# Kernel tuning notes

Measured on AMD Instinct MI355X. Metric: run time of the kernel, lower is better.

## Reference

```python
import jax, jax.numpy as jnp
import numpy as np

N_LAYERS = 8
D_MODEL = 64
D_STATE = 32
D_CONV = 4
D_INNER = 128          # expand * d_model
HEADDIM = 64
NHEADS = D_INNER // HEADDIM      # 2
CONV_DIM = D_INNER + 2 * D_STATE # 192 (x, B, C)
D_IN_PROJ = 2 * D_INNER + 2 * D_STATE + NHEADS  # 322
EPS = 1e-5


def setup_inputs() -> dict:
    key = jax.random.key(0)
    ks = jax.random.split(key, 8)
    x = jax.random.normal(ks[0], (16, 4096, D_MODEL), dtype=jnp.float32)
    Win = jax.random.normal(ks[1], (N_LAYERS, D_MODEL, D_IN_PROJ), dtype=jnp.float32) * 0.05
    conv_w = jax.random.normal(ks[2], (N_LAYERS, CONV_DIM, D_CONV), dtype=jnp.float32) * 0.2
    conv_b = jnp.zeros((N_LAYERS, CONV_DIM), dtype=jnp.float32)
    dt_bias = jax.random.uniform(ks[3], (N_LAYERS, NHEADS), minval=-4.0, maxval=-1.0)
    A_log = jnp.log(jax.random.uniform(ks[4], (N_LAYERS, NHEADS), minval=1.0, maxval=16.0))
    Dp = jnp.ones((N_LAYERS, NHEADS), dtype=jnp.float32)
    norm_w = jnp.ones((N_LAYERS, D_INNER), dtype=jnp.float32)
    Wout = jax.random.normal(ks[5], (N_LAYERS, D_INNER, D_MODEL), dtype=jnp.float32) * 0.05
    return {"x": x, "Win": Win, "conv_w": conv_w, "conv_b": conv_b,
            "dt_bias": dt_bias, "A_log": A_log, "Dp": Dp,
            "norm_w": norm_w, "Wout": Wout}


def _mamba2_layer(u, Win, conv_w, conv_b, dt_bias, A_log, Dp, norm_w, Wout):
    b, l, _ = u.shape
    zxbcdt = u @ Win                                   # (b,l,322)
    z = zxbcdt[..., :D_INNER]                          # gate (b,l,128)
    xBC = zxbcdt[..., D_INNER:D_INNER + CONV_DIM]      # (b,l,192)
    dt = jax.nn.softplus(zxbcdt[..., D_INNER + CONV_DIM:] + dt_bias)  # (b,l,H)

    # causal depthwise conv over time, then SiLU
    xc = jnp.pad(xBC.transpose(0, 2, 1), ((0, 0), (0, 0), (D_CONV - 1, 0)))
    xc = jax.lax.conv_general_dilated(
        xc, conv_w[:, None, :], (1,), 'VALID',
        feature_group_count=CONV_DIM,
        dimension_numbers=('NCH', 'OIH', 'NCH'))
    xBC = jax.nn.silu((xc + conv_b[None, :, None]).transpose(0, 2, 1))  # (b,l,192)

    xs = xBC[..., :D_INNER].reshape(b, l, NHEADS, HEADDIM)   # (b,l,h,p)
    B = xBC[..., D_INNER:D_INNER + D_STATE]                  # (b,l,n)
    C = xBC[..., D_INNER + D_STATE:]                         # (b,l,n)

    A = -jnp.exp(A_log)                                      # (h,) negative
    dA = jnp.exp(dt * A)                                     # (b,l,h)

    # sequential selective scan over time; state (b,h,p,n)
    def step(hst, inp):
        dA_t, dt_t, x_t, B_t, C_t = inp
        hst = hst * dA_t[:, :, None, None] + \
              (dt_t[:, :, None] * x_t)[..., None] * B_t[:, None, None, :]
        y_t = jnp.einsum('bhpn,bn->bhp', hst, C_t)
        return hst, y_t

    h0 = jnp.zeros((b, NHEADS, HEADDIM, D_STATE), dtype=u.dtype)
    seq = (jnp.moveaxis(dA, 1, 0), jnp.moveaxis(dt, 1, 0),
           jnp.moveaxis(xs, 1, 0), jnp.moveaxis(B, 1, 0), jnp.moveaxis(C, 1, 0))
    _, ys = jax.lax.scan(step, h0, seq)                      # (l,b,h,p)
    y = jnp.moveaxis(ys, 0, 1) + Dp[None, None, :, None] * xs  # (b,l,h,p)
    y = y.reshape(b, l, D_INNER)

    # gated RMSNorm (norm_before_gate=False): normalize after gating
    y = y * jax.nn.silu(z)
    y = y * jax.lax.rsqrt(jnp.mean(y * y, axis=-1, keepdims=True) + EPS) * norm_w
    return y @ Wout                                          # (b,l,d_model)


def reference(x, Win, conv_w, conv_b, dt_bias, A_log, Dp, norm_w, Wout):
    h = x
    for i in range(N_LAYERS - 1):
        h = _mamba2_layer(h, Win[i], conv_w[i], conv_b[i], dt_bias[i],
                          A_log[i], Dp[i], norm_w[i], Wout[i])
    h = jax.lax.stop_gradient(h)  # layers[:-1] run under torch.no_grad()
    i = N_LAYERS - 1
    return _mamba2_layer(h, Win[i], conv_w[i], conv_b[i], dt_bias[i],
                         A_log[i], Dp[i], norm_w[i], Wout[i])
```

## Files before the change

### kernel.cpp

```cpp
#include <hip/hip_runtime.h>
#include <math.h>

#define BATCH   16
#define SEQ     4096
#define DMODEL  64
#define DINNER  128
#define DSTATE  32
#define NHEADS  2
#define HEADDIM 64
#define CONVDIM 192
#define PROJ    322
#define QC      64
#define NCHUNK  (SEQ/QC)
#define BL      (BATCH*SEQ)
#define NPAD    336

typedef __attribute__((ext_vector_type(8))) short short8;
typedef __attribute__((ext_vector_type(4))) float f32x4;

__device__ inline unsigned short f2b(float f){
  union { float f; unsigned u; } v; v.f = f;
  unsigned r = v.u + 0x7FFF + ((v.u >> 16) & 1);
  return (unsigned short)(r >> 16);
}
__device__ inline float b2f(unsigned short s){
  union { unsigned u; float f; } v; v.u = ((unsigned)s) << 16; return v.f;
}
__device__ inline void split2(float x, unsigned short& h, unsigned short& l){
  unsigned short hh = f2b(x);
  h = hh;
  l = f2b(x - b2f(hh));
}

__device__ float g_z   [(size_t)BL*DINNER];
__device__ float g_xbc [(size_t)BL*CONVDIM];
__device__ float g_y   [(size_t)BL*DINNER];
__device__ unsigned short g_C[(size_t)BL*DSTATE];
__device__ float g_dt  [BATCH*NHEADS*SEQ];
__device__ float g_cum [BATCH*NHEADS*SEQ];
__device__ float g_ctot[BATCH*NHEADS*NCHUNK];
__device__ float g_S   [BATCH*NHEADS*NCHUNK*DSTATE*HEADDIM];
__device__ float g_H   [BATCH*NHEADS*NCHUNK*DSTATE*HEADDIM];
__device__ float g_ping0[(size_t)BL*DMODEL];
__device__ float g_ping1[(size_t)BL*DMODEL];
__device__ unsigned short g_WinTh [8*NPAD*DMODEL];
__device__ unsigned short g_WinTl [8*NPAD*DMODEL];
__device__ unsigned short g_WoutTh[8*DMODEL*DINNER];
__device__ unsigned short g_WoutTl[8*DMODEL*DINNER];

__global__ __launch_bounds__(256) void k_prep(const float* __restrict__ Win,
                                              const float* __restrict__ Wout,
                                              const float* __restrict__ normw) {
  const int idx = blockIdx.x*256 + threadIdx.x;
  const int NW = 8*NPAD*DMODEL;
  if (idx < NW) {
    int layer = idx / (NPAD*DMODEL);
    int rem   = idx - layer*(NPAD*DMODEL);
    int n = rem >> 6, k = rem & 63;
    float v = (n < PROJ) ? Win[(size_t)layer*DMODEL*PROJ + k*PROJ + n] : 0.f;
    split2(v, g_WinTh[idx], g_WinTl[idx]);
  } else {
    int i2 = idx - NW;
    if (i2 < 8*DMODEL*DINNER) {
      int layer = i2 / (DMODEL*DINNER);
      int rem   = i2 - layer*(DMODEL*DINNER);
      int n = rem >> 7, k = rem & 127;
      float v = Wout[(size_t)layer*DINNER*DMODEL + k*DMODEL + n] * normw[layer*DINNER + k];
      split2(v, g_WoutTh[i2], g_WoutTl[i2]);
    }
  }
}

__global__ __launch_bounds__(256) void k_inproj(const float* __restrict__ xext, int sel,
                                                const unsigned short* __restrict__ WinTh,
                                                const unsigned short* __restrict__ WinTl,
                                                const float* __restrict__ Win,
                                                const float* __restrict__ dt_bias,
                                                const float* __restrict__ A_log) {
  __shared__ float stgAll[4][16][68];
  const float* __restrict__ X = (sel==0) ? xext : (sel==1 ? g_ping0 : g_ping1);
  const int bx = blockIdx.x;
  const int chunk = bx >> 1, half = bx & 1;
  const int row0 = chunk * 64;
  const int tid = threadIdx.x;
  const int w = tid>>6, l = tid&63, lane15 = l&15, quad = l>>4;

  const float* xrow = &X[(size_t)(row0 + 16*w + lane15)*DMODEL + quad*8];
  float4 f0 = *(const float4*)(xrow);
  float4 f1 = *(const float4*)(xrow + 4);
  float4 f2 = *(const float4*)(xrow + 32);
  float4 f3 = *(const float4*)(xrow + 36);

  if (half==0 && w < 2) {
    const int h = w, t = l;
    float acc = 0.f;
    const float* xr = &X[(size_t)(row0+t)*DMODEL];
#pragma unroll
    for (int k=0;k<64;k++) acc = fmaf(xr[k], Win[k*PROJ + (DINNER+CONVDIM) + h], acc);
    float xv = acc + dt_bias[h];
    float dtv = (xv > 20.f) ? xv : log1pf(expf(xv));
    float A = -expf(A_log[h]);
    float cum = dtv * A;
#pragma unroll
    for (int off=1; off<64; off<<=1){
      float v = __shfl_up(cum, off);
      if (t >= off) cum += v;
    }
    const int b = chunk>>6, ch = chunk&63;
    const int base = (b*NHEADS + h)*SEQ + ch*QC + t;
    g_dt [base] = dtv;
    g_cum[base] = cum;
    if (t == 63) g_ctot[(b*NHEADS+h)*NCHUNK + ch] = cum;
  }

  short8 a0h, a0l, a1h, a1l;
  {
    float v0[8] = {f0.x,f0.y,f0.z,f0.w,f1.x,f1.y,f1.z,f1.w};
    float v1[8] = {f2.x,f2.y,f2.z,f2.w,f3.x,f3.y,f3.z,f3.w};
    unsigned short hh, ll;
#pragma unroll
    for (int j=0;j<8;j++){ split2(v0[j], hh, ll); a0h[j]=(short)hh; a0l[j]=(short)ll; }
#pragma unroll
    for (int j=0;j<8;j++){ split2(v1[j], hh, ll); a1h[j]=(short)hh; a1l[j]=(short)ll; }
  }

  float (*stg)[68] = stgAll[w];
  const int gS = (half==0) ? 0 : 2;
  const int gE = (half==0) ? 2 : 5;
#pragma unroll 1
  for (int g5=gS; g5<gE; g5++){
    f32x4 acc4[4];
#pragma unroll
    for (int tt=0; tt<4; tt++){
      int t = g5*4 + tt;
      const unsigned short* bph = &WinTh[(16*t + lane15)*64 + quad*8];
      const unsigned short* bpl = &WinTl[(16*t + lane15)*64 + quad*8];
      short8 b0h = *(const short8*)bph;
      short8 b1h = *(const short8*)(bph + 32);
      short8 b0l = *(const short8*)bpl;
      short8 b1l = *(const short8*)(bpl + 32);
      f32x4 acc = {0.f,0.f,0.f,0.f};
      acc = __builtin_amdgcn_mfma_f32_16x16x32_bf16(a0h, b0h, acc, 0, 0, 0);
      acc = __builtin_amdgcn_mfma_f32_16x16x32_bf16(a1h, b1h, acc, 0, 0, 0);
      acc = __builtin_amdgcn_mfma_f32_16x16x32_bf16(a0l, b0h, acc, 0, 0, 0);
      acc = __builtin_amdgcn_mfma_f32_16x16x32_bf16(a1l, b1h, acc, 0, 0, 0);
      acc = __builtin_amdgcn_mfma_f32_16x16x32_bf16(a0h, b0l, acc, 0, 0, 0);
      acc = __builtin_amdgcn_mfma_f32_16x16x32_bf16(a1h, b1l, acc, 0, 0, 0);
      acc4[tt] = acc;
    }
#pragma unroll
    for (int tt=0; tt<4; tt++)
#pragma unroll
      for (int r=0;r<4;r++)
        stg[quad*4+r][tt*16+lane15] = acc4[tt][r];
#pragma unroll
    for (int it=0; it<4; it++){
      int e = it*64 + l;
      int lr = e>>4, c4 = (e&15)<<2;
      float4 v = *(const float4*)&stg[lr][c4];
      size_t grow = row0 + 16*w + lr;
      int gcol = g5*64 + c4;
      if (g5 < 2) *(float4*)&g_z  [grow*DINNER  + gcol]          = v;
      else        *(float4*)&g_xbc[grow*CONVDIM + gcol - DINNER] = v;
    }
  }
}

__global__ __launch_bounds__(256,4) void k_chunkA(const float* __restrict__ conv_w,
                                                  const float* __restrict__ conv_b,
                                                  const float* __restrict__ Dp) {
  __shared__ float Xf[64][66];
  __shared__ unsigned short Xt [64][72];
  __shared__ unsigned short Bt [32][72];
  union BCG {
    struct { unsigned short Bsh[64][40]; unsigned short Csh[64][40]; } bc;
    unsigned short Gsh[64][72];
  };
  __shared__ BCG u;
  const int bx = blockIdx.x; const int b = bx>>7, h=(bx>>6)&1, ch=bx&63;
  const int tid = threadIdx.x;
  const size_t row0 = (size_t)b*SEQ + (size_t)ch*QC;
  const int cbase = (b*NHEADS+h)*SEQ + ch*QC;
  const float dph = Dp[h];
  if (tid < QC){
    float cl = g_cum[cbase+63];
    float cu = g_cum[cbase+tid], dtv = g_dt[cbase+tid];
    Xf[tid][64] = cu;
    Xf[tid][65] = dtv;
    ((float*)&Bt[tid>>1][64])[tid&1] = expf(cl - cu) * dtv;
  }
  const int cc = tid & 127, half = tid >> 7, t0 = half*32;
  const int gch = (cc < 64) ? (h*64 + cc) : (64 + cc);
  const float w0 = conv_w[gch*4+0], w1 = conv_w[gch*4+1], w2 = conv_w[gch*4+2], w3 = conv_w[gch*4+3];
  const float bb = conv_b[gch];
  float v0, v1, v2;
  if (ch==0 && half==0){ v0=0.f; v1=0.f; v2=0.f; }
  else {
    v0 = g_xbc[(row0+t0-3)*CONVDIM + gch];
    v1 = g_xbc[(row0+t0-2)*CONVDIM + gch];
    v2 = g_xbc[(row0+t0-1)*CONVDIM + gch];
  }
  __syncthreads();
  if (cc < 64){
#pragma unroll
    for (int blk=0; blk<4; ++blk){
      unsigned short xb[8];
#pragma unroll
      for (int j=0;j<8;j++){
        int t = t0 + blk*8 + j;
        float v3 = g_xbc[(row0+t)*CONVDIM + gch];
        float a = fmaf(w0,v0, fmaf(w1,v1, fmaf(w2,v2, fmaf(w3,v3, bb))));
        float sv = a / (1.f + expf(-a));
        Xf[cc][t] = sv;
        xb[j] = f2b(sv);
        v0=v1; v1=v2; v2=v3;
      }
      *(short8*)&Xt[cc][t0 + blk*8] = *(const short8*)xb;
    }
  } else if (cc < 96){
    const int n = cc - 64;
#pragma unroll
    for (int blk=0; blk<4; ++blk){
      unsigned short bt8[8];
#pragma unroll
      for (int j=0;j<8;j++){
        int t = t0 + blk*8 + j;
        float v3 = g_xbc[(row0+t)*CONVDIM + gch];
        float a = fmaf(w0,v0, fmaf(w1,v1, fmaf(w2,v2, fmaf(w3,v3, bb))));
        float sv = a / (1.f + expf(-a));
        u.bc.Bsh[t][n] = f2b(sv);
        float ew = ((const float*)&Bt[t>>1][64])[t&1];
        bt8[j] = f2b(sv * ew);
        v0=v1; v1=v2; v2=v3;
      }
      *(short8*)&Bt[n][t0 + blk*8] = *(const short8*)bt8;
    }
  } else {
    const int n = cc - 96;
#pragma unroll 4
    for (int t=t0; t<t0+32; t++){
      float v3 = g_xbc[(row0+t)*CONVDIM + gch];
      float a = fmaf(w0,v0, fmaf(w1,v1, fmaf(w2,v2, fmaf(w3,v3, bb))));
      float sv = a / (1.f + expf(-a));
      u.bc.Csh[t][n] = f2b(sv);
      if (h == 0) g_C[(row0+t)*DSTATE + n] = f2b(sv);
      v0=v1; v1=v2; v2=v3;
    }
  }
  __syncthreads();
  const int w = tid>>6, l = tid&63, lane15 = l&15, quad = l>>4;
  short8 afr = *(const short8*)&u.bc.Csh[16*w + lane15][quad*8];
  f32x4 gacc[4];
#pragma unroll
  for (int tn=0;tn<4;tn++){
    short8 bfr = *(const short8*)&u.bc.Bsh[16*tn + lane15][quad*8];
    f32x4 z = {0.f,0.f,0.f,0.f};
    gacc[tn] = __builtin_amdgcn_mfma_f32_16x16x32_bf16(afr, bfr, z, 0, 0, 0);
  }
  __syncthreads();
#pragma unroll
  for (int tn=0;tn<4;tn++){
    int s = 16*tn + lane15;
    float cs = Xf[s][64], ds = Xf[s][65];
#pragma unroll
    for (int r=0;r<4;r++){
      int t = 16*w + quad*4 + r;
      float gv = 0.f;
      if (s <= t) gv = expf(Xf[t][64]-cs) * ds * gacc[tn][r];
      u.Gsh[t][s] = f2b(gv);
    }
  }
  __syncthreads();
#pragma unroll
  for (int tn=0;tn<4;tn++){
    f32x4 acc = {0.f,0.f,0.f,0.f};
#pragma unroll
    for (int ks=0;ks<2;ks++){
      short8 a  = *(const short8*)&u.Gsh[16*w  + lane15][quad*8 + 32*ks];
      short8 bf = *(const short8*)&Xt [16*tn + lane15][quad*8 + 32*ks];
      acc = __builtin_amdgcn_mfma_f32_16x16x32_bf16(a, bf, acc, 0, 0, 0);
    }
    int p = 16*tn + lane15;
#pragma unroll
    for (int r=0;r<4;r++){
      int t = 16*w + quad*4 + r;
      g_y[(row0+t)*DINNER + h*HEADDIM + p] = acc[r] + dph * Xf[p][t];
    }
  }
  const size_t sb = (size_t)((b*NHEADS+h)*NCHUNK + ch) * (DSTATE*HEADDIM);
  const int tm2 = w & 1, tnb = (w>>1)*2;
#pragma unroll
  for (int tt=0;tt<2;tt++){
    int tn2 = tnb + tt;
    f32x4 acc = {0.f,0.f,0.f,0.f};
#pragma unroll
    for (int ks=0;ks<2;ks++){
      short8 a  = *(const short8*)&Bt[16*tm2 + lane15][quad*8 + 32*ks];
      short8 bf = *(const short8*)&Xt[16*tn2 + lane15][quad*8 + 32*ks];
      acc = __builtin_amdgcn_mfma_f32_16x16x32_bf16(a, bf, acc, 0, 0, 0);
    }
    int p = 16*tn2 + lane15;
#pragma unroll
    for (int r=0;r<4;r++){
      int n = 16*tm2 + quad*4 + r;
      g_S[sb + n*HEADDIM + p] = acc[r];
    }
  }
}

__global__ __launch_bounds__(256) void k_chunkScan() {
  __shared__ float dAc[NCHUNK];
  const int idx = blockIdx.x*256 + threadIdx.x;
  const int np = idx & 2047;
  const int bh = idx >> 11;
  if (threadIdx.x < NCHUNK) dAc[threadIdx.x] = expf(g_ctot[bh*NCHUNK + threadIdx.x]);
  __syncthreads();
  float h = 0.f;
  const size_t base = (size_t)bh*NCHUNK*2048 + np;
#pragma unroll 1
  for (int k0=0; k0<NCHUNK; k0+=8){
    float s[8];
#pragma unroll
    for (int j=0;j<8;j++) s[j] = g_S[base + (size_t)(k0+j)*2048];
    float hs[8];
#pragma unroll
    for (int j=0;j<8;j++){
      hs[j] = h;
      h = h*dAc[k0+j] + s[j];
    }
#pragma unroll
    for (int j=0;j<8;j++) g_H[base + (size_t)(k0+j)*2048] = hs[j];
  }
}

__global__ __launch_bounds__(256,3) void k_fusedC(const unsigned short* __restrict__ WoutTh,
                                                  const unsigned short* __restrict__ WoutTl,
                                                  float* __restrict__ dout, int dsel) {
  __shared__ float Cl[QC][DSTATE+1];
  __shared__ float ec[NHEADS][QC];
  __shared__ unsigned short yAh[64][136];
  __shared__ unsigned short yAl[64][136];
  float* __restrict__ out = (dsel==0) ? g_ping0 : (dsel==1 ? g_ping1 : dout);
  const int bx = blockIdx.x; const int b = bx>>6, ch = bx&63;
  const int tid = threadIdx.x;
  const size_t row0 = (size_t)b*SEQ + (size_t)ch*QC;
  const int w = tid>>6, l = tid&63, lane15 = l&15, quad = l>>4;
#pragma unroll
  for (int j=0;j<8;j++){ int e=tid+j*256; int s=e>>5, n=e&31;
    Cl[s][n] = b2f(g_C[(row0+s)*DSTATE + n]); }
  if (tid < 128){ int h_=tid>>6, s=tid&63;
    ec[h_][s] = expf(g_cum[(b*NHEADS+h_)*SEQ + ch*QC + s]); }
  float hr[64];
  {
    const float* H0 = &g_H[(size_t)((b*NHEADS+0)*NCHUNK + ch)*2048];
    const float* H1 = &g_H[(size_t)((b*NHEADS+1)*NCHUNK + ch)*2048];
#pragma unroll
    for (int n=0;n<32;n++){ hr[n] = H0[n*64 + l]; hr[32+n] = H1[n*64 + l]; }
  }
  __syncthreads();
#pragma unroll 1
  for (int i=0;i<16;i++){
    const int r = 16*w + i;
    const size_t row = row0 + r;
    float d0 = 0.f, d1 = 0.f;
#pragma unroll
    for (int n=0;n<32;n++){
      float c = Cl[r][n];
      d0 = fmaf(c, hr[n],    d0);
      d1 = fmaf(c, hr[32+n], d1);
    }
    float yv0 = g_y[row*DINNER + l]      + ec[0][r]*d0;
    float yv1 = g_y[row*DINNER + l + 64] + ec[1][r]*d1;
    float z0 = g_z[row*DINNER + l];
    float z1 = g_z[row*DINNER + l + 64];
    yv0 *= z0 / (1.f + expf(-z0));
    yv1 *= z1 / (1.f + expf(-z1));
    float ss = yv0*yv0 + yv1*yv1;
#pragma unroll
    for (int off=32; off>=1; off>>=1) ss += __shfl_xor(ss, off);
    float sc = rsqrtf(ss*(1.f/128.f) + 1e-5f);
    split2(yv0*sc, yAh[r][l],    yAl[r][l]);
    split2(yv1*sc, yAh[r][l+64], yAl[r][l+64]);
  }
  __syncthreads();
  short8 afh[4], afl[4];
#pragma unroll
  for (int ks=0;ks<4;ks++){
    afh[ks] = *(const short8*)&yAh[16*w + lane15][quad*8 + 32*ks];
    afl[ks] = *(const short8*)&yAl[16*w + lane15][quad*8 + 32*ks];
  }
  __syncthreads();
  float (*stgF)[68] = (float(*)[68])((float*)&yAh[0][0] + (size_t)w*16*68);
#pragma unroll
  for (int tc=0;tc<4;tc++){
    f32x4 acc = {0.f,0.f,0.f,0.f};
#pragma unroll
    for (int ks=0;ks<4;ks++){
      const unsigned short* bph = &WoutTh[(16*tc + lane15)*DINNER + quad*8 + 32*ks];
      const unsigned short* bpl = &WoutTl[(16*tc + lane15)*DINNER + quad*8 + 32*ks];
      short8 bh  = *(const short8*)bph;
      short8 blo = *(const short8*)bpl;
      acc = __builtin_amdgcn_mfma_f32_16x16x32_bf16(afh[ks], bh,  acc, 0, 0, 0);
      acc = __builtin_amdgcn_mfma_f32_16x16x32_bf16(afl[ks], bh,  acc, 0, 0, 0);
      acc = __builtin_amdgcn_mfma_f32_16x16x32_bf16(afh[ks], blo, acc, 0, 0, 0);
    }
#pragma unroll
    for (int r=0;r<4;r++)
      stgF[quad*4+r][tc*16+lane15] = acc[r];
  }
#pragma unroll
  for (int it=0; it<4; it++){
    int e = it*64 + l;
    int lr = e>>4, c4 = (e&15)<<2;
    float4 v = *(const float4*)&stgF[lr][c4];
    *(float4*)&out[(row0 + 16*w + lr)*DMODEL + c4] = v;
  }
}

extern "C" void kernel_launch(void* const* d_in, const int* in_sizes, int n_in,
                              void* d_out, int out_size, void* d_ws, size_t ws_size,
                              hipStream_t stream) {
  (void)in_sizes; (void)n_in; (void)d_ws; (void)ws_size; (void)out_size;
  const float* x       = (const float*)d_in[0];
  const float* Win     = (const float*)d_in[1];
  const float* conv_w  = (const float*)d_in[2];
  const float* conv_b  = (const float*)d_in[3];
  const float* dt_bias = (const float*)d_in[4];
  const float* A_log   = (const float*)d_in[5];
  const float* Dp      = (const float*)d_in[6];
  const float* norm_w  = (const float*)d_in[7];
  const float* Wout    = (const float*)d_in[8];

  k_prep<<<(8*(NPAD*DMODEL + DMODEL*DINNER) + 255)/256, 256, 0, stream>>>(Win, Wout, norm_w);

  unsigned short *winTh, *winTl, *woutTh, *woutTl;
  hipGetSymbolAddress((void**)&winTh,  HIP_SYMBOL(g_WinTh));
  hipGetSymbolAddress((void**)&winTl,  HIP_SYMBOL(g_WinTl));
  hipGetSymbolAddress((void**)&woutTh, HIP_SYMBOL(g_WoutTh));
  hipGetSymbolAddress((void**)&woutTl, HIP_SYMBOL(g_WoutTl));

  for (int layer = 0; layer < 8; ++layer) {
    const int insel = (layer==0) ? 0 : ((((layer-1)&1)==0) ? 1 : 2);
    const int dsel  = (layer==7) ? 2 : ((layer&1)==0 ? 0 : 1);

    k_inproj<<<(BL/64)*2, 256, 0, stream>>>(x, insel,
                                        winTh + (size_t)layer*NPAD*DMODEL,
                                        winTl + (size_t)layer*NPAD*DMODEL,
                                        Win + (size_t)layer*DMODEL*PROJ,
                                        dt_bias + layer*NHEADS, A_log + layer*NHEADS);
    k_chunkA<<<BATCH*NHEADS*NCHUNK, 256, 0, stream>>>(conv_w + (size_t)layer*CONVDIM*4,
                                                      conv_b + (size_t)layer*CONVDIM,
                                                      Dp + layer*NHEADS);
    k_chunkScan<<<(BATCH*NHEADS*DSTATE*HEADDIM)/256, 256, 0, stream>>>();
    k_fusedC<<<BATCH*NCHUNK, 256, 0, stream>>>(woutTh + (size_t)layer*DMODEL*DINNER,
                                               woutTl + (size_t)layer*DMODEL*DINNER,
                                               (float*)d_out, dsel);
  }
}
```

Baseline: 1.275 ms.

## Fuse input projection into chunk kernel, recomputing conv halo to drop xBC buffer

Merges the in-projection GEMM with the conv/chunk-state kernel, so each (batch, head, chunk) block computes its own x/B/C projection slices into shared memory. The 3-row conv halo is taken from the previous chunk by recomputing a 16-row projection tile. This removes the global round trip through the g_xbc buffer and one kernel launch. In exchange, B/C and the halo rows are recomputed per head, occupancy drops to 2 blocks per CU, and shared memory use grows.

```diff
diff --git a/kernel.cpp b/kernel.cpp
--- a/kernel.cpp
+++ b/kernel.cpp
@@ -33,7 +33,6 @@
 }
 
 __device__ float g_z   [(size_t)BL*DINNER];
-__device__ float g_xbc [(size_t)BL*CONVDIM];
 __device__ float g_y   [(size_t)BL*DINNER];
 __device__ unsigned short g_C[(size_t)BL*DSTATE];
 __device__ float g_dt  [BATCH*NHEADS*SEQ];
@@ -71,104 +70,16 @@
   }
 }
 
-__global__ __launch_bounds__(256) void k_inproj(const float* __restrict__ xext, int sel,
-                                                const unsigned short* __restrict__ WinTh,
-                                                const unsigned short* __restrict__ WinTl,
-                                                const float* __restrict__ Win,
-                                                const float* __restrict__ dt_bias,
-                                                const float* __restrict__ A_log) {
-  __shared__ float stgAll[4][16][68];
-  const float* __restrict__ X = (sel==0) ? xext : (sel==1 ? g_ping0 : g_ping1);
-  const int bx = blockIdx.x;
-  const int chunk = bx >> 1, half = bx & 1;
-  const int row0 = chunk * 64;
-  const int tid = threadIdx.x;
-  const int w = tid>>6, l = tid&63, lane15 = l&15, quad = l>>4;
-
-  const float* xrow = &X[(size_t)(row0 + 16*w + lane15)*DMODEL + quad*8];
-  float4 f0 = *(const float4*)(xrow);
-  float4 f1 = *(const float4*)(xrow + 4);
-  float4 f2 = *(const float4*)(xrow + 32);
-  float4 f3 = *(const float4*)(xrow + 36);
-
-  if (half==0 && w < 2) {
-    const int h = w, t = l;
-    float acc = 0.f;
-    const float* xr = &X[(size_t)(row0+t)*DMODEL];
-#pragma unroll
-    for (int k=0;k<64;k++) acc = fmaf(xr[k], Win[k*PROJ + (DINNER+CONVDIM) + h], acc);
-    float xv = acc + dt_bias[h];
-    float dtv = (xv > 20.f) ? xv : log1pf(expf(xv));
-    float A = -expf(A_log[h]);
-    float cum = dtv * A;
-#pragma unroll
-    for (int off=1; off<64; off<<=1){
-      float v = __shfl_up(cum, off);
-      if (t >= off) cum += v;
-    }
-    const int b = chunk>>6, ch = chunk&63;
-    const int base = (b*NHEADS + h)*SEQ + ch*QC + t;
-    g_dt [base] = dtv;
-    g_cum[base] = cum;
-    if (t == 63) g_ctot[(b*NHEADS+h)*NCHUNK + ch] = cum;
-  }
-
-  short8 a0h, a0l, a1h, a1l;
-  {
-    float v0[8] = {f0.x,f0.y,f0.z,f0.w,f1.x,f1.y,f1.z,f1.w};
-    float v1[8] = {f2.x,f2.y,f2.z,f2.w,f3.x,f3.y,f3.z,f3.w};
-    unsigned short hh, ll;
-#pragma unroll
-    for (int j=0;j<8;j++){ split2(v0[j], hh, ll); a0h[j]=(short)hh; a0l[j]=(short)ll; }
-#pragma unroll
-    for (int j=0;j<8;j++){ split2(v1[j], hh, ll); a1h[j]=(short)hh; a1l[j]=(short)ll; }
-  }
-
-  float (*stg)[68] = stgAll[w];
-  const int gS = (half==0) ? 0 : 2;
-  const int gE = (half==0) ? 2 : 5;
-#pragma unroll 1
-  for (int g5=gS; g5<gE; g5++){
-    f32x4 acc4[4];
-#pragma unroll
-    for (int tt=0; tt<4; tt++){
-      int t = g5*4 + tt;
-      const unsigned short* bph = &WinTh[(16*t + lane15)*64 + quad*8];
-      const unsigned short* bpl = &WinTl[(16*t + lane15)*64 + quad*8];
-      short8 b0h = *(const short8*)bph;
-      short8 b1h = *(const short8*)(bph + 32);
-      short8 b0l = *(const short8*)bpl;
-      short8 b1l = *(const short8*)(bpl + 32);
-      f32x4 acc = {0.f,0.f,0.f,0.f};
-      acc = __builtin_amdgcn_mfma_f32_16x16x32_bf16(a0h, b0h, acc, 0, 0, 0);
-      acc = __builtin_amdgcn_mfma_f32_16x16x32_bf16(a1h, b1h, acc, 0, 0, 0);
-      acc = __builtin_amdgcn_mfma_f32_16x16x32_bf16(a0l, b0h, acc, 0, 0, 0);
-      acc = __builtin_amdgcn_mfma_f32_16x16x32_bf16(a1l, b1h, acc, 0, 0, 0);
-      acc = __builtin_amdgcn_mfma_f32_16x16x32_bf16(a0h, b0l, acc, 0, 0, 0);
-      acc = __builtin_amdgcn_mfma_f32_16x16x32_bf16(a1h, b1l, acc, 0, 0, 0);
-      acc4[tt] = acc;
-    }
-#pragma unroll
-    for (int tt=0; tt<4; tt++)
-#pragma unroll
-      for (int r=0;r<4;r++)
-        stg[quad*4+r][tt*16+lane15] = acc4[tt][r];
-#pragma unroll
-    for (int it=0; it<4; it++){
-      int e = it*64 + l;
-      int lr = e>>4, c4 = (e&15)<<2;
-      float4 v = *(const float4*)&stg[lr][c4];
-      size_t grow = row0 + 16*w + lr;
-      int gcol = g5*64 + c4;
-      if (g5 < 2) *(float4*)&g_z  [grow*DINNER  + gcol]          = v;
-      else        *(float4*)&g_xbc[grow*CONVDIM + gcol - DINNER] = v;
-    }
-  }
-}
-
-__global__ __launch_bounds__(256,4) void k_chunkA(const float* __restrict__ conv_w,
-                                                  const float* __restrict__ conv_b,
-                                                  const float* __restrict__ Dp) {
+__global__ __launch_bounds__(256,2) void k_fusedAB(const float* __restrict__ xext, int sel,
+                                                   const unsigned short* __restrict__ WinTh,
+                                                   const unsigned short* __restrict__ WinTl,
+                                                   const float* __restrict__ Win,
+                                                   const float* __restrict__ dt_bias,
+                                                   const float* __restrict__ A_log,
+                                                   const float* __restrict__ conv_w,
+                                                   const float* __restrict__ conv_b,
+                                                   const float* __restrict__ Dp) {
+  __shared__ float PC[80][66];
   __shared__ float Xf[64][66];
   __shared__ unsigned short Xt [64][72];
   __shared__ unsigned short Bt [32][72];
@@ -177,38 +88,115 @@
     unsigned short Gsh[64][72];
   };
   __shared__ BCG u;
-  const int bx = blockIdx.x; const int b = bx>>7, h=(bx>>6)&1, ch=bx&63;
+
+  const float* __restrict__ X = (sel==0) ? xext : (sel==1 ? g_ping0 : g_ping1);
+  const int bx = blockIdx.x; const int b = bx>>7, h = (bx>>6)&1, ch = bx&63;
   const int tid = threadIdx.x;
+  const int w = tid>>6, l = tid&63, lane15 = l&15, quad = l>>4;
   const size_t row0 = (size_t)b*SEQ + (size_t)ch*QC;
   const int cbase = (b*NHEADS+h)*SEQ + ch*QC;
   const float dph = Dp[h];
-  if (tid < QC){
-    float cl = g_cum[cbase+63];
-    float cu = g_cum[cbase+tid], dtv = g_dt[cbase+tid];
-    Xf[tid][64] = cu;
-    Xf[tid][65] = dtv;
-    ((float*)&Bt[tid>>1][64])[tid&1] = expf(cl - cu) * dtv;
-  }
-  const int cc = tid & 127, half = tid >> 7, t0 = half*32;
-  const int gch = (cc < 64) ? (h*64 + cc) : (64 + cc);
-  const float w0 = conv_w[gch*4+0], w1 = conv_w[gch*4+1], w2 = conv_w[gch*4+2], w3 = conv_w[gch*4+3];
-  const float bb = conv_b[gch];
-  float v0, v1, v2;
-  if (ch==0 && half==0){ v0=0.f; v1=0.f; v2=0.f; }
-  else {
-    v0 = g_xbc[(row0+t0-3)*CONVDIM + gch];
-    v1 = g_xbc[(row0+t0-2)*CONVDIM + gch];
-    v2 = g_xbc[(row0+t0-1)*CONVDIM + gch];
-  }
-  __syncthreads();
-  if (cc < 64){
-#pragma unroll
-    for (int blk=0; blk<4; ++blk){
+
+  const float* xrow = &X[(row0 + 16*w + lane15)*DMODEL + quad*8];
+  float4 f0 = *(const float4*)(xrow);
+  float4 f1 = *(const float4*)(xrow + 4);
+  float4 f2 = *(const float4*)(xrow + 32);
+  float4 f3 = *(const float4*)(xrow + 36);
+  short8 a0h, a0l, a1h, a1l;
+  {
+    float v0[8] = {f0.x,f0.y,f0.z,f0.w,f1.x,f1.y,f1.z,f1.w};
+    float v1[8] = {f2.x,f2.y,f2.z,f2.w,f3.x,f3.y,f3.z,f3.w};
+    unsigned short hh, ll;
+#pragma unroll
+    for (int j=0;j<8;j++){ split2(v0[j], hh, ll); a0h[j]=(short)hh; a0l[j]=(short)ll; }
+#pragma unroll
+    for (int j=0;j<8;j++){ split2(v1[j], hh, ll); a1h[j]=(short)hh; a1l[j]=(short)ll; }
+  }
+  short8 e0h, e0l, e1h, e1l;
+  if (ch != 0){
+    const float* xh = &X[(row0 - 16 + lane15)*DMODEL + quad*8];
+    float4 g0 = *(const float4*)(xh);
+    float4 g1 = *(const float4*)(xh + 4);
+    float4 g2 = *(const float4*)(xh + 32);
+    float4 g3 = *(const float4*)(xh + 36);
+    float v0[8] = {g0.x,g0.y,g0.z,g0.w,g1.x,g1.y,g1.z,g1.w};
+    float v1[8] = {g2.x,g2.y,g2.z,g2.w,g3.x,g3.y,g3.z,g3.w};
+    unsigned short hh, ll;
+#pragma unroll
+    for (int j=0;j<8;j++){ split2(v0[j], hh, ll); e0h[j]=(short)hh; e0l[j]=(short)ll; }
+#pragma unroll
+    for (int j=0;j<8;j++){ split2(v1[j], hh, ll); e1h[j]=(short)hh; e1l[j]=(short)ll; }
+  }
+
+  if (w == 0) {
+    const int t = l;
+    float acc = 0.f;
+    const float* xr = &X[(row0+t)*DMODEL];
+#pragma unroll
+    for (int k=0;k<64;k++) acc = fmaf(xr[k], Win[k*PROJ + (DINNER+CONVDIM) + h], acc);
+    float xv = acc + dt_bias[h];
+    float dtv = (xv > 20.f) ? xv : log1pf(expf(xv));
+    float A = -expf(A_log[h]);
+    float cum = dtv * A;
+#pragma unroll
+    for (int off=1; off<64; off<<=1){
+      float v = __shfl_up(cum, off);
+      if (t >= off) cum += v;
+    }
+    g_dt [cbase+t] = dtv;
+    g_cum[cbase+t] = cum;
+    if (t == 63) g_ctot[(b*NHEADS+h)*NCHUNK + ch] = cum;
+    float cl = __shfl(cum, 63);
+    Xf[t][64] = cum;
+    Xf[t][65] = dtv;
+    ((float*)&Bt[t>>1][64])[t&1] = expf(cl - cum) * dtv;
+  }
+
+  auto MFMA6 = [&](short8 A0h, short8 A1h, short8 A0l, short8 A1l, int t)->f32x4 {
+    const unsigned short* bph = &WinTh[(16*t + lane15)*64 + quad*8];
+    const unsigned short* bpl = &WinTl[(16*t + lane15)*64 + quad*8];
+    short8 b0h = *(const short8*)bph;
+    short8 b1h = *(const short8*)(bph + 32);
+    short8 b0l = *(const short8*)bpl;
+    short8 b1l = *(const short8*)(bpl + 32);
+    f32x4 acc = {0.f,0.f,0.f,0.f};
+    acc = __builtin_amdgcn_mfma_f32_16x16x32_bf16(A0h, b0h, acc, 0, 0, 0);
+    acc = __builtin_amdgcn_mfma_f32_16x16x32_bf16(A1h, b1h, acc, 0, 0, 0);
+    acc = __builtin_amdgcn_mfma_f32_16x16x32_bf16(A0l, b0h, acc, 0, 0, 0);
+    acc = __builtin_amdgcn_mfma_f32_16x16x32_bf16(A1l, b1h, acc, 0, 0, 0);
+    acc = __builtin_amdgcn_mfma_f32_16x16x32_bf16(A0h, b0l, acc, 0, 0, 0);
+    acc = __builtin_amdgcn_mfma_f32_16x16x32_bf16(A1h, b1l, acc, 0, 0, 0);
+    return acc;
+  };
+
+#pragma unroll
+  for (int tt=0; tt<4; tt++){
+    f32x4 acc = MFMA6(a0h, a1h, a0l, a1l, 8+4*h+tt);
+#pragma unroll
+    for (int r=0;r<4;r++) PC[16 + 16*w + quad*4 + r][tt*16 + lane15] = acc[r];
+  }
+  if (ch != 0){
+    f32x4 acc = MFMA6(e0h, e1h, e0l, e1l, 8+4*h+w);
+#pragma unroll
+    for (int r=0;r<4;r++) PC[quad*4 + r][w*16 + lane15] = acc[r];
+  } else if (tid < 192) {
+    PC[13 + (tid>>6)][tid & 63] = 0.f;
+  }
+  __syncthreads();
+
+  {
+    const int cc = l, t0 = w*16;
+    const int gch = h*64 + cc;
+    const float w0 = conv_w[gch*4+0], w1 = conv_w[gch*4+1], w2 = conv_w[gch*4+2], w3 = conv_w[gch*4+3];
+    const float bb = conv_b[gch];
+    float v0 = PC[16+t0-3][cc], v1 = PC[16+t0-2][cc], v2 = PC[16+t0-1][cc];
+#pragma unroll
+    for (int blk=0; blk<2; ++blk){
       unsigned short xb[8];
 #pragma unroll
       for (int j=0;j<8;j++){
         int t = t0 + blk*8 + j;
-        float v3 = g_xbc[(row0+t)*CONVDIM + gch];
+        float v3 = PC[16+t][cc];
         float a = fmaf(w0,v0, fmaf(w1,v1, fmaf(w2,v2, fmaf(w3,v3, bb))));
         float sv = a / (1.f + expf(-a));
         Xf[cc][t] = sv;
@@ -217,38 +205,65 @@
       }
       *(short8*)&Xt[cc][t0 + blk*8] = *(const short8*)xb;
     }
-  } else if (cc < 96){
-    const int n = cc - 64;
-#pragma unroll
-    for (int blk=0; blk<4; ++blk){
-      unsigned short bt8[8];
-#pragma unroll
-      for (int j=0;j<8;j++){
-        int t = t0 + blk*8 + j;
-        float v3 = g_xbc[(row0+t)*CONVDIM + gch];
+  }
+  __syncthreads();
+
+#pragma unroll
+  for (int tt=0; tt<4; tt++){
+    f32x4 acc = MFMA6(a0h, a1h, a0l, a1l, 16+tt);
+#pragma unroll
+    for (int r=0;r<4;r++) PC[16 + 16*w + quad*4 + r][tt*16 + lane15] = acc[r];
+  }
+  if (ch != 0){
+    f32x4 acc = MFMA6(e0h, e1h, e0l, e1l, 16+w);
+#pragma unroll
+    for (int r=0;r<4;r++) PC[quad*4 + r][w*16 + lane15] = acc[r];
+  } else if (tid < 192) {
+    PC[13 + (tid>>6)][tid & 63] = 0.f;
+  }
+  __syncthreads();
+
+  {
+    const int cc = l, t0 = w*16;
+    if (cc < 32){
+      const int n = cc, gch = 128 + cc;
+      const float w0 = conv_w[gch*4+0], w1 = conv_w[gch*4+1], w2 = conv_w[gch*4+2], w3 = conv_w[gch*4+3];
+      const float bb = conv_b[gch];
+      float v0 = PC[16+t0-3][cc], v1 = PC[16+t0-2][cc], v2 = PC[16+t0-1][cc];
+#pragma unroll
+      for (int blk=0; blk<2; ++blk){
+        unsigned short bt8[8];
+#pragma unroll
+        for (int j=0;j<8;j++){
+          int t = t0 + blk*8 + j;
+          float v3 = PC[16+t][cc];
+          float a = fmaf(w0,v0, fmaf(w1,v1, fmaf(w2,v2, fmaf(w3,v3, bb))));
+          float sv = a / (1.f + expf(-a));
+          u.bc.Bsh[t][n] = f2b(sv);
+          float ew = ((const float*)&Bt[t>>1][64])[t&1];
+          bt8[j] = f2b(sv * ew);
+          v0=v1; v1=v2; v2=v3;
+        }
+        *(short8*)&Bt[n][t0 + blk*8] = *(const short8*)bt8;
+      }
+    } else {
+      const int n = cc - 32, gch = 160 + n;
+      const float w0 = conv_w[gch*4+0], w1 = conv_w[gch*4+1], w2 = conv_w[gch*4+2], w3 = conv_w[gch*4+3];
+      const float bb = conv_b[gch];
+      float v0 = PC[16+t0-3][cc], v1 = PC[16+t0-2][cc], v2 = PC[16+t0-1][cc];
+#pragma unroll 4
+      for (int t=t0; t<t0+16; t++){
+        float v3 = PC[16+t][cc];
         float a = fmaf(w0,v0, fmaf(w1,v1, fmaf(w2,v2, fmaf(w3,v3, bb))));
         float sv = a / (1.f + expf(-a));
-        u.bc.Bsh[t][n] = f2b(sv);
-        float ew = ((const float*)&Bt[t>>1][64])[t&1];
-        bt8[j] = f2b(sv * ew);
+        u.bc.Csh[t][n] = f2b(sv);
+        if (h == 0) g_C[(row0+t)*DSTATE + n] = f2b(sv);
         v0=v1; v1=v2; v2=v3;
       }
-      *(short8*)&Bt[n][t0 + blk*8] = *(const short8*)bt8;
-    }
-  } else {
-    const int n = cc - 96;
-#pragma unroll 4
-    for (int t=t0; t<t0+32; t++){
-      float v3 = g_xbc[(row0+t)*CONVDIM + gch];
-      float a = fmaf(w0,v0, fmaf(w1,v1, fmaf(w2,v2, fmaf(w3,v3, bb))));
-      float sv = a / (1.f + expf(-a));
-      u.bc.Csh[t][n] = f2b(sv);
-      if (h == 0) g_C[(row0+t)*DSTATE + n] = f2b(sv);
-      v0=v1; v1=v2; v2=v3;
-    }
-  }
-  __syncthreads();
-  const int w = tid>>6, l = tid&63, lane15 = l&15, quad = l>>4;
+    }
+  }
+  __syncthreads();
+
   short8 afr = *(const short8*)&u.bc.Csh[16*w + lane15][quad*8];
   f32x4 gacc[4];
 #pragma unroll
@@ -304,6 +319,25 @@
     for (int r=0;r<4;r++){
       int n = 16*tm2 + quad*4 + r;
       g_S[sb + n*HEADDIM + p] = acc[r];
+    }
+  }
+
+  {
+    float (*stg)[66] = (float(*)[66])&PC[20*w][0];
+    f32x4 acc4[4];
+#pragma unroll
+    for (int tt=0; tt<4; tt++) acc4[tt] = MFMA6(a0h, a1h, a0l, a1l, 4*h+tt);
+#pragma unroll
+    for (int tt=0; tt<4; tt++)
+#pragma unroll
+      for (int r=0;r<4;r++)
+        stg[quad*4+r][tt*16+lane15] = acc4[tt][r];
+#pragma unroll
+    for (int it=0; it<4; it++){
+      int e = it*64 + l;
+      int lr = e>>4, c4 = (e&15)<<2;
+      float4 v = *(const float4*)&stg[lr][c4];
+      *(float4*)&g_z[(row0 + 16*w + lr)*DINNER + h*64 + c4] = v;
     }
   }
 }
@@ -443,14 +477,14 @@
     const int insel = (layer==0) ? 0 : ((((layer-1)&1)==0) ? 1 : 2);
     const int dsel  = (layer==7) ? 2 : ((layer&1)==0 ? 0 : 1);
 
-    k_inproj<<<(BL/64)*2, 256, 0, stream>>>(x, insel,
+    k_fusedAB<<<BATCH*NHEADS*NCHUNK, 256, 0, stream>>>(x, insel,
                                         winTh + (size_t)layer*NPAD*DMODEL,
                                         winTl + (size_t)layer*NPAD*DMODEL,
                                         Win + (size_t)layer*DMODEL*PROJ,
-                                        dt_bias + layer*NHEADS, A_log + layer*NHEADS);
-    k_chunkA<<<BATCH*NHEADS*NCHUNK, 256, 0, stream>>>(conv_w + (size_t)layer*CONVDIM*4,
-                                                      conv_b + (size_t)layer*CONVDIM,
-                                                      Dp + layer*NHEADS);
+                                        dt_bias + layer*NHEADS, A_log + layer*NHEADS,
+                                        conv_w + (size_t)layer*CONVDIM*4,
+                                        conv_b + (size_t)layer*CONVDIM,
+                                        Dp + layer*NHEADS);
     k_chunkScan<<<(BATCH*NHEADS*DSTATE*HEADDIM)/256, 256, 0, stream>>>();
     k_fusedC<<<BATCH*NCHUNK, 256, 0, stream>>>(woutTh + (size_t)layer*DMODEL*DINNER,
                                                woutTl + (size_t)layer*DMODEL*DINNER,
```

Measured after the change: 1.272 ms. No clear change (-0.2%).
